# Performance work log

Hardware: AMD Instinct MI355X
Metric: run time of the kernel (lower is better)

## Reference

```python
import jax, jax.numpy as jnp
import numpy as np

B, P, K, KS = 512, 64, 30, 4      # graphs, nodes per graph, sort-pool k, conv1d kernel
N, E, F, H = B * P, 524288, 128, 256
N_CLASSES = 10
L_OUT = K - KS + 1                 # 27, conv1d output length


def _sage(h, wl, wr, b, src, dst, inv_deg):
    # PyG SAGEConv (mean aggr): out = lin_l(mean_j x_j) + lin_r(x_i); bias only on lin_l
    agg = jax.ops.segment_sum(h[src], dst, num_segments=N) * inv_deg
    return jax.nn.relu(agg @ wl + b + h @ wr)


def setup_inputs() -> dict:
    key = jax.random.key(0)
    ks = jax.random.split(key, 32)
    x = jax.random.normal(ks[0], (N, F), jnp.float32)
    # intra-graph random edges (src -> dst aggregation)
    g = jax.random.randint(ks[1], (E,), 0, B)
    src = g * P + jax.random.randint(ks[2], (E,), 0, P)
    dst = g * P + jax.random.randint(ks[3], (E,), 0, P)
    edge_index = jnp.stack([src, dst]).astype(jnp.int32)
    batch = jnp.repeat(jnp.arange(B), P).astype(jnp.int32)  # sorted graph ids

    def lin(k, i, o):
        return jax.random.normal(k, (i, o), jnp.float32) / np.float32(np.sqrt(i))

    inp = {"x": x, "edge_index": edge_index, "batch": batch}
    dims = [(F, H), (H, H), (H, H), (H, H)]
    ki = 4
    for li, (i, o) in enumerate(dims):
        inp[f"sage{li}_wl"] = lin(ks[ki], i, o); ki += 1
        inp[f"sage{li}_wr"] = lin(ks[ki], i, o); ki += 1
        inp[f"sage{li}_b"] = jnp.zeros((o,), jnp.float32)
    inp["conv1d_w"] = jax.random.normal(ks[ki], (H, H, KS), jnp.float32) / np.float32(np.sqrt(H * KS)); ki += 1
    inp["conv1d_b"] = jnp.zeros((H,), jnp.float32)
    inp["lin1_w"] = lin(ks[ki], H * L_OUT, H); ki += 1
    inp["lin1_b"] = jnp.zeros((H,), jnp.float32)
    inp["lin2_w"] = lin(ks[ki], H, 128); ki += 1
    inp["lin2_b"] = jnp.zeros((128,), jnp.float32)
    inp["out_w"] = lin(ks[ki], 128, N_CLASSES); ki += 1
    inp["out_b"] = jnp.zeros((N_CLASSES,), jnp.float32)
    return inp


def reference(x, edge_index, batch,
              sage0_wl, sage0_wr, sage0_b,
              sage1_wl, sage1_wr, sage1_b,
              sage2_wl, sage2_wr, sage2_b,
              sage3_wl, sage3_wr, sage3_b,
              conv1d_w, conv1d_b, lin1_w, lin1_b,
              lin2_w, lin2_b, out_w, out_b):
    src, dst = edge_index[0], edge_index[1]
    deg = jax.ops.segment_sum(jnp.ones(src.shape, x.dtype), dst, num_segments=N)
    inv_deg = (1.0 / jnp.maximum(deg, 1.0))[:, None]

    h = jnp.nan_to_num(x, nan=0.0)
    h = _sage(h, sage0_wl, sage0_wr, sage0_b, src, dst, inv_deg)
    h = _sage(h, sage1_wl, sage1_wr, sage1_b, src, dst, inv_deg)
    h = _sage(h, sage2_wl, sage2_wr, sage2_b, src, dst, inv_deg)
    h = _sage(h, sage3_wl, sage3_wr, sage3_b, src, dst, inv_deg)  # [N, H]

    # SortAggregation(k=K): to dense batch, sort by last channel desc, top-k, zero-pad
    counts = jax.ops.segment_sum(jnp.ones(N, jnp.int32), batch, num_segments=B)
    offsets = jnp.cumsum(counts) - counts
    pos = jnp.arange(N) - offsets[batch]
    D = h.shape[1]
    dense = jnp.zeros((B, P, D), h.dtype).at[batch, pos].set(h)
    valid = jnp.zeros((B, P), bool).at[batch, pos].set(True)
    skey = jnp.where(valid, dense[..., -1], -jnp.inf)
    order = jnp.argsort(-skey, axis=1)[:, :K]                       # [B, K]
    topk = jnp.take_along_axis(dense, order[..., None], axis=1)     # [B, K, D]
    tvalid = jnp.take_along_axis(valid, order, axis=1)
    topk = jnp.where(tvalid[..., None], topk, 0.0)

    # x.view(B, K, -1).permute(0, 2, 1) -> [B, D, K]
    xc = topk.transpose(0, 2, 1)
    y = jax.lax.conv_general_dilated(xc, conv1d_w, (1,), 'VALID',
                                     dimension_numbers=('NCH', 'OIH', 'NCH'))
    y = jax.nn.relu(y + conv1d_b[None, :, None])                    # [B, H, L_OUT]
    y = y.reshape(B, -1)                                            # dropout is identity in eval
    y = jax.nn.relu(y @ lin1_w + lin1_b)
    y = jax.nn.relu(y @ lin2_w + lin2_b)
    return jax.nn.relu(y @ out_w + out_b)                           # [B, N_CLASSES]
```

## Files before the change

### kernel.cpp

```cpp
#include <hip/hip_runtime.h>
#include <hip/hip_bf16.h>

#define NNODES 32768
#define NEDGES 524288
#define NGRAPH 512
#define PNODES 64
#define KTOP 30
#define FIN 128
#define HID 256
#define LOUT 27

#define C1F 4.8828125e-4f
#define C2F 2.384185791015625e-7f

using f16x8 = __attribute__((ext_vector_type(8))) _Float16;
using f16x4 = __attribute__((ext_vector_type(4))) _Float16;
using f32x4 = __attribute__((ext_vector_type(4))) float;
using f32x16 = __attribute__((ext_vector_type(16))) float;

#define GLDS(src, dst) __builtin_amdgcn_global_load_lds( \
    (const __attribute__((address_space(1))) void*)(src), \
    (__attribute__((address_space(3))) void*)(dst), 16, 0, 0)

__global__ void hist_kernel(const int* __restrict__ dst, int* __restrict__ counts) {
    int e = blockIdx.x * blockDim.x + threadIdx.x;
    if (e < NEDGES) atomicAdd(&counts[dst[e]], 1);
}

__global__ __launch_bounds__(1024) void scan_block_kernel(const int* __restrict__ counts,
        int* __restrict__ loc, int* __restrict__ partial) {
    int b = blockIdx.x, t = threadIdx.x;
    int i = b * 1024 + t;
    int v = counts[i];
    int lane = t & 63, w = t >> 6;
    int x = v;
    #pragma unroll
    for (int d = 1; d < 64; d <<= 1) { int y = __shfl_up(x, d, 64); if (lane >= d) x += y; }
    __shared__ int ws[16];
    if (lane == 63) ws[w] = x;
    __syncthreads();
    if (w == 0) {
        int s = (lane < 16) ? ws[lane] : 0;
        #pragma unroll
        for (int d = 1; d < 16; d <<= 1) { int y = __shfl_up(s, d, 64); if (lane >= d) s += y; }
        if (lane < 16) ws[lane] = s;
    }
    __syncthreads();
    int base = (w > 0) ? ws[w - 1] : 0;
    int incl = base + x;
    loc[i] = incl - v;
    if (t == 1023) partial[b] = incl;
}

__global__ __launch_bounds__(1024) void scan_fixup_kernel(const int* __restrict__ loc,
        const int* __restrict__ partial, const int* __restrict__ counts,
        int* __restrict__ offsets, int* __restrict__ cursor, float* __restrict__ invdeg) {
    int b = blockIdx.x, t = threadIdx.x;
    int i = b * 1024 + t;
    __shared__ int sbase;
    if (t == 0) { int s = 0; for (int j = 0; j < b; ++j) s += partial[j]; sbase = s; }
    __syncthreads();
    int o = loc[i] + sbase;
    offsets[i] = o;
    cursor[i] = o;
    invdeg[i] = 1.0f / fmaxf((float)counts[i], 1.0f);
}

__global__ void scatter_kernel(const int* __restrict__ src, const int* __restrict__ dst,
        int* __restrict__ cursor, int* __restrict__ ssrc) {
    int e = blockIdx.x * blockDim.x + threadIdx.x;
    if (e < NEDGES) {
        int d = dst[e];
        int p = atomicAdd(&cursor[d], 1);
        ssrc[p] = ((d & 63) << 6) | (src[e] & 63);
    }
}

__global__ void nan2num_split_kernel(const float* __restrict__ x,
        _Float16* __restrict__ oh, _Float16* __restrict__ ol, int n4) {
    int i = blockIdx.x * blockDim.x + threadIdx.x;
    if (i >= n4) return;
    float4 v = *(const float4*)(x + i * 4);
    float xs[4] = {v.x, v.y, v.z, v.w};
    f16x4 hh, ll;
    #pragma unroll
    for (int q = 0; q < 4; ++q) {
        float a = xs[q];
        a = (a != a) ? 0.f : a;
        _Float16 h = (_Float16)a;
        hh[q] = h;
        ll[q] = (_Float16)((a - (float)h) * 2048.0f);
    }
    *(f16x4*)(oh + (size_t)i * 4) = hh;
    *(f16x4*)(ol + (size_t)i * 4) = ll;
}

struct PrepSage {
    const float* src[8];
    _Float16* dh[8];
    _Float16* dl[8];
    int logK[8];
    int part[8];
};

__global__ __launch_bounds__(256) void prep_sage_kernel(PrepSage p) {
    int y = blockIdx.y;
    int idx = blockIdx.x * 256 + threadIdx.x;
    int lk = p.logK[y], K = 1 << lk;
    if (idx >= 256 * K) return;
    int n = idx >> lk, k = idx & (K - 1);
    float w = p.src[y][(size_t)k * 256 + n];
    _Float16 h = (_Float16)w;
    int wv = n >> 5, l31 = n & 31;
    int c = k >> 5, h2 = (k >> 4) & 1, hb = (k >> 3) & 1, j = k & 7;
    int NCH = K >> 5;
    size_t dst = (size_t)(wv * 2 + p.part[y]) * (size_t)(NCH * 1024)
               + (size_t)(c * 2 + h2) * 512 + (size_t)(hb * 32 + l31) * 8 + j;
    p.dh[y][dst] = h;
    p.dl[y][dst] = (_Float16)((w - (float)h) * 2048.0f);
}

__global__ __launch_bounds__(256) void prep_conv_kernel(const float* __restrict__ W,
        _Float16* __restrict__ b0, _Float16* __restrict__ b1) {
    int idx = blockIdx.x * 256 + threadIdx.x;
    int o = idx >> 10, k = idx & 1023;
    float w = W[(size_t)o * 1024 + (k & 255) * 4 + (k >> 8)];
    _Float16 h = (_Float16)w;
    b0[(size_t)o * 1024 + k] = h;
    b1[(size_t)o * 1024 + k] = (_Float16)((w - (float)h) * 2048.0f);
}

__global__ __launch_bounds__(256) void prep_lin1_kernel(const float* __restrict__ l1w,
        _Float16* __restrict__ wh, _Float16* __restrict__ wl_) {
    __shared__ float sh[64][65];
    int kb = blockIdx.x * 64;
    int nb = blockIdx.y * 64;
    int t = threadIdx.x;
    {
        int kk = t >> 2;
        int nc = (t & 3) * 16;
        int k = kb + kk, l = k >> 8, c = k & 255;
        const float* srow = l1w + (size_t)(c * 27 + l) * 256 + nb + nc;
        #pragma unroll
        for (int j = 0; j < 16; j += 4) {
            float4 v = *(const float4*)(srow + j);
            sh[kk][nc + j + 0] = v.x;
            sh[kk][nc + j + 1] = v.y;
            sh[kk][nc + j + 2] = v.z;
            sh[kk][nc + j + 3] = v.w;
        }
    }
    __syncthreads();
    {
        int nn = t >> 2;
        int kc = (t & 3) * 16;
        f16x8 oh[2], ol[2];
        #pragma unroll
        for (int j = 0; j < 16; ++j) {
            float x = sh[kc + j][nn];
            _Float16 h = (_Float16)x;
            oh[j >> 3][j & 7] = h;
            ol[j >> 3][j & 7] = (_Float16)((x - (float)h) * 2048.0f);
        }
        size_t o = (size_t)(nb + nn) * 6912 + kb + kc;
        *(f16x8*)(wh + o) = oh[0];
        *(f16x8*)(wh + o + 8) = oh[1];
        *(f16x8*)(wl_ + o) = ol[0];
        *(f16x8*)(wl_ + o + 8) = ol[1];
    }
}

template<int HIN>
__global__ __launch_bounds__(512, 4) void fused_sage3_kernel(
        const _Float16* __restrict__ hh, const _Float16* __restrict__ hl,
        const int* __restrict__ offsets, const int* __restrict__ counts,
        const int* __restrict__ ssrc, const float* __restrict__ invdeg,
        const _Float16* __restrict__ Wsh, const _Float16* __restrict__ Wsl,
        const float* __restrict__ bias,
        _Float16* __restrict__ outh, _Float16* __restrict__ outl) {
    constexpr int NCH = HIN / 32;
    __shared__ __align__(16) _Float16 hp[2][NCH * 2048];
    __shared__ __align__(16) uint32_t Sw[4096];
    const int g = blockIdx.x, t = threadIdx.x;
    const int lane = t & 63, wave = t >> 6;
    const int l31 = lane & 31, hb = lane >> 5;
    const size_t gbase = (size_t)g * 64 * HIN;

    #pragma unroll
    for (int i = 0; i < 8; ++i) Sw[t + i * 512] = 0;

    {
        int a = lane >> 2, b = lane & 3;
        for (int u = wave; u < NCH * 8; u += 8) {
            int part = u & 1;
            int cs = u >> 1;
            int c = cs >> 2, stripe = cs & 3;
            int row = stripe * 16 + a;
            int o = b ^ ((row >> 1) & 3) ^ (c & 3);
            const _Float16* src = (part ? hl : hh) + gbase + (size_t)row * HIN + c * 32 + o * 8;
            GLDS(src, &hp[part][c * 2048 + stripe * 512]);
        }
    }

    const int gbeg = offsets[g * 64];
    const int gend = offsets[g * 64 + 63] + counts[g * 64 + 63];
    __syncthreads();

    for (int e = gbeg + t; e < gend; e += 512)
        atomicAdd(&Sw[ssrc[e] & 4095], 1u);
    __syncthreads();

    {
        int d = t >> 3, o = t & 7;
        float idg = invdeg[g * 64 + d];
        float v[8];
        #pragma unroll
        for (int j = 0; j < 8; ++j) v[j] = (float)Sw[(d << 6) + (o << 3) + j] * idg;
        __syncthreads();
        _Float16* Sp = (_Float16*)Sw;
        f16x8 s0, s1;
        #pragma unroll
        for (int j = 0; j < 8; ++j) {
            _Float16 h1 = (_Float16)v[j];
            s0[j] = h1;
            s1[j] = (_Float16)((v[j] - (float)h1) * 2048.0f);
        }
        int addr = (d << 6) + ((o ^ (d & 7)) << 3);
        *(f16x8*)&Sp[addr] = s0;
        *(f16x8*)&Sp[4096 + addr] = s1;
    }
    __syncthreads();

    const int col = (wave << 5) + l31;

    auto gemmKV = [&](int part, f32x16* a0, f32x16* a1) {
        const _Float16* __restrict__ Bh = Wsh + (size_t)((wave << 1) + part) * (size_t)(NCH * 1024);
        const _Float16* __restrict__ Bl = Wsl + (size_t)((wave << 1) + part) * (size_t)(NCH * 1024);
        #pragma unroll 2
        for (int c = 0; c < NCH; ++c) {
            #pragma unroll
            for (int h2 = 0; h2 < 2; ++h2) {
                f16x8 ah[2], al_[2];
                #pragma unroll
                for (int mi = 0; mi < 2; ++mi) {
                    int row = (mi << 5) + l31;
                    int slot = (2 * h2 + hb) ^ ((row >> 1) & 3) ^ (c & 3);
                    int addr = c * 2048 + (row << 5) + (slot << 3);
                    ah[mi] = *(const f16x8*)&hp[0][addr];
                    al_[mi] = *(const f16x8*)&hp[1][addr];
                }
                int ko = ((c << 1) + h2) * 512 + (lane << 3);
                f16x8 bh = *(const f16x8*)(Bh + ko);
                f16x8 bl = *(const f16x8*)(Bl + ko);
                #pragma unroll
                for (int mi = 0; mi < 2; ++mi) {
                    a0[mi] = __builtin_amdgcn_mfma_f32_32x32x16_f16(ah[mi], bh, a0[mi], 0, 0, 0);
                    a1[mi] = __builtin_amdgcn_mfma_f32_32x32x16_f16(al_[mi], bh, a1[mi], 0, 0, 0);
                    a1[mi] = __builtin_amdgcn_mfma_f32_32x32x16_f16(ah[mi], bl, a1[mi], 0, 0, 0);
                }
            }
        }
    };

    f32x16 acc0[2], acc1[2];
    acc0[0] = 0.f; acc0[1] = 0.f; acc1[0] = 0.f; acc1[1] = 0.f;
    gemmKV(0, acc0, acc1);
    f32x16 pf[2];
    pf[0] = acc0[0] + C1F * acc1[0];
    pf[1] = acc0[1] + C1F * acc1[1];

    f32x16 so0[2], so1[2];
    so0[0] = 0.f; so0[1] = 0.f; so1[0] = 0.f; so1[1] = 0.f;
    {
        const _Float16* Sp = (const _Float16*)Sw;
        #pragma unroll
        for (int kc = 0; kc < 4; ++kc) {
            float kv[4], sv[4];
            #pragma unroll
            for (int j = 0; j < 4; ++j) {
                float e0 = pf[(2 * kc) >> 2][((2 * kc) & 3) * 4 + j];
                float e1 = pf[(2 * kc + 1) >> 2][((2 * kc + 1) & 3) * 4 + j];
                kv[j] = hb ? e1 : e0;
                sv[j] = hb ? e0 : e1;
            }
            uint32_t kh[2], kl2[2], sh_[2], sl2[2];
            #pragma unroll
            for (int q = 0; q < 2; ++q) {
                union { uint32_t u; _Float16 f[2]; } H1, L1, H2, L2;
                #pragma unroll
                for (int j = 0; j < 2; ++j) {
                    float x = kv[q * 2 + j];
                    _Float16 h1 = (_Float16)x;
                    H1.f[j] = h1; L1.f[j] = (_Float16)((x - (float)h1) * 2048.0f);
                    float y = sv[q * 2 + j];
                    _Float16 h2 = (_Float16)y;
                    H2.f[j] = h2; L2.f[j] = (_Float16)((y - (float)h2) * 2048.0f);
                }
                kh[q] = H1.u; kl2[q] = L1.u; sh_[q] = H2.u; sl2[q] = L2.u;
            }
            uint32_t rh0 = (uint32_t)__shfl_xor((int)sh_[0], 32, 64);
            uint32_t rh1 = (uint32_t)__shfl_xor((int)sh_[1], 32, 64);
            uint32_t rl0 = (uint32_t)__shfl_xor((int)sl2[0], 32, 64);
            uint32_t rl1 = (uint32_t)__shfl_xor((int)sl2[1], 32, 64);
            union { uint32_t u[4]; f16x8 v; } bh_, bl_;
            bh_.u[0] = hb ? rh0 : kh[0];  bh_.u[1] = hb ? rh1 : kh[1];
            bh_.u[2] = hb ? kh[0] : rh0;  bh_.u[3] = hb ? kh[1] : rh1;
            bl_.u[0] = hb ? rl0 : kl2[0]; bl_.u[1] = hb ? rl1 : kl2[1];
            bl_.u[2] = hb ? kl2[0] : rl0; bl_.u[3] = hb ? kl2[1] : rl1;
            #pragma unroll
            for (int mi = 0; mi < 2; ++mi) {
                int row = (mi << 5) + l31;
                int soff = (row << 6) + (((2 * kc + hb) ^ (row & 7)) << 3);
                f16x8 s0f = *(const f16x8*)&Sp[soff];
                f16x8 s1f = *(const f16x8*)&Sp[4096 + soff];
                so0[mi] = __builtin_amdgcn_mfma_f32_32x32x16_f16(s0f, bh_.v, so0[mi], 0, 0, 0);
                so1[mi] = __builtin_amdgcn_mfma_f32_32x32x16_f16(s0f, bl_.v, so1[mi], 0, 0, 0);
                so1[mi] = __builtin_amdgcn_mfma_f32_32x32x16_f16(s1f, bh_.v, so1[mi], 0, 0, 0);
            }
        }
    }
    f32x16 sC[2];
    sC[0] = so0[0] + C1F * so1[0];
    sC[1] = so0[1] + C1F * so1[1];

    acc0[0] = 0.f; acc0[1] = 0.f; acc1[0] = 0.f; acc1[1] = 0.f;
    gemmKV(1, acc0, acc1);

    const float bb = bias[col];
    #pragma unroll
    for (int mi = 0; mi < 2; ++mi)
        #pragma unroll
        for (int reg = 0; reg < 16; ++reg)
            sC[mi][reg] = fmaxf(sC[mi][reg] + acc0[mi][reg] + C1F * acc1[mi][reg] + bb, 0.f);

    __syncthreads();
    _Float16* eL = &hp[0][0];
    #pragma unroll
    for (int part = 0; part < 2; ++part) {
        #pragma unroll
        for (int mi = 0; mi < 2; ++mi) {
            #pragma unroll
            for (int reg = 0; reg < 16; ++reg) {
                int row = (mi << 5) + (reg & 3) + ((reg >> 2) << 3) + (hb << 2);
                int cx = col ^ ((((row >> 2) & 1) << 5) | ((row & 3) << 3));
                float v = sC[mi][reg];
                _Float16 h1 = (_Float16)v;
                eL[(row << 8) + cx] = part ? (_Float16)((v - (float)h1) * 2048.0f) : h1;
            }
        }
        __syncthreads();
        _Float16* gout = part ? outl : outh;
        #pragma unroll
        for (int it = 0; it < 4; ++it) {
            int i = (t << 3) + (it << 12);
            int row = i >> 8, cc = i & 255;
            int sx = cc ^ ((((row >> 2) & 1) << 5) | ((row & 3) << 3));
            f16x8 v8 = *(const f16x8*)&eL[(row << 8) + sx];
            *(f16x8*)(gout + (size_t)((g << 6) + row) * HID + cc) = v8;
        }
        if (part == 0) __syncthreads();
    }
}

template<int NPROD, int CONV, int NPAIRS, int EPI>
__global__ __launch_bounds__(256, 2) void mfma_ps_kernel(
        const _Float16* __restrict__ A1h, const _Float16* __restrict__ A1l,
        const _Float16* __restrict__ A2h, const _Float16* __restrict__ A2l,
        const _Float16* __restrict__ B1h, const _Float16* __restrict__ B1l,
        const _Float16* __restrict__ B2h, const _Float16* __restrict__ B2l,
        const float* __restrict__ bias,
        _Float16* __restrict__ outh, _Float16* __restrict__ outl,
        float* __restrict__ Cpart,
        int lda, int K, int Nd, int nrb) {
    __shared__ _Float16 As[2][2][128 * 32];
    __shared__ _Float16 Bs[2][2][128 * 32];
    const int t = threadIdx.x;
    const int lane = t & 63, wave = t >> 6;
    const int wr = wave & 1, wc = wave >> 1;
    const int bid = blockIdx.x;
    const int rb = bid % nrb, cb = bid / nrb;
    const int row0 = rb * 128, col0 = cb * 128;
    const int l31 = lane & 31, hb = lane >> 5, x3 = l31 & 3;
    const int r16 = lane >> 2;
    const int qsrc8 = ((lane & 3) ^ (r16 & 3)) * 8;
    size_t aoffj[2], boffj[2];
    #pragma unroll
    for (int j = 0; j < 2; ++j) {
        int ar = row0 + wave * 32 + j * 16 + r16;
        aoffj[j] = CONV ? ((size_t)ar * 256 + (size_t)(ar / 27) * 768)
                        : (size_t)ar * (size_t)lda;
        boffj[j] = (size_t)(col0 + wave * 32 + j * 16 + r16) * (size_t)K;
    }
    int aroff[2], broff[2], slot8[2];
    #pragma unroll
    for (int mi = 0; mi < 2; ++mi) aroff[mi] = (wr * 64 + mi * 32 + l31) * 32;
    #pragma unroll
    for (int ni = 0; ni < 2; ++ni) broff[ni] = (wc * 64 + ni * 32 + l31) * 32;
    #pragma unroll
    for (int h = 0; h < 2; ++h) slot8[h] = ((2 * h + hb) ^ x3) * 8;

    const int KV = NPAIRS * K;
    const int kchunk = KV / gridDim.z;
    const int kv_lo = blockIdx.z * kchunk, kv_hi = kv_lo + kchunk;

    f32x16 acc0[2][2], acc1[2][2], acc2[2][2];
    #pragma unroll
    for (int i = 0; i < 2; ++i)
        #pragma unroll
        for (int j = 0; j < 2; ++j) { acc0[i][j] = 0.f; acc1[i][j] = 0.f; acc2[i][j] = 0.f; }

    auto stage = [&](int kv, int b) {
        int p = (NPAIRS == 2 && kv >= K) ? 1 : 0;
        int k = kv - p * K;
        const _Float16* __restrict__ sAh = p ? A2h : A1h;
        const _Float16* __restrict__ sAl = p ? A2l : A1l;
        const _Float16* __restrict__ sBh = p ? B2h : B1h;
        const _Float16* __restrict__ sBl = p ? B2l : B1l;
        #pragma unroll
        for (int j = 0; j < 2; ++j) {
            int ldsbase = (wave * 32 + j * 16) * 32;
            size_t ga = aoffj[j] + k + qsrc8;
            size_t gb = boffj[j] + k + qsrc8;
            GLDS(sAh + ga, &As[b][0][ldsbase]);
            GLDS(sAl + ga, &As[b][1][ldsbase]);
            GLDS(sBh + gb, &Bs[b][0][ldsbase]);
            GLDS(sBl + gb, &Bs[b][1][ldsbase]);
        }
    };

    stage(kv_lo, 0);
    __syncthreads();
    int b = 0;
    for (int kv = kv_lo; kv < kv_hi; kv += 32) {
        if (kv + 32 < kv_hi) stage(kv + 32, b ^ 1);
        #pragma unroll
        for (int h = 0; h < 2; ++h) {
            f16x8 af0[2], af1[2], bf0[2], bf1[2];
            #pragma unroll
            for (int mi = 0; mi < 2; ++mi) {
                af0[mi] = *(const f16x8*)&As[b][0][aroff[mi] + slot8[h]];
                af1[mi] = *(const f16x8*)&As[b][1][aroff[mi] + slot8[h]];
            }
            #pragma unroll
            for (int ni = 0; ni < 2; ++ni) {
                bf0[ni] = *(const f16x8*)&Bs[b][0][broff[ni] + slot8[h]];
                bf1[ni] = *(const f16x8*)&Bs[b][1][broff[ni] + slot8[h]];
            }
            #pragma unroll
            for (int mi = 0; mi < 2; ++mi)
                #pragma unroll
                for (int ni = 0; ni < 2; ++ni) {
                    acc0[mi][ni] = __builtin_amdgcn_mfma_f32_32x32x16_f16(af0[mi], bf0[ni], acc0[mi][ni], 0, 0, 0);
                    acc1[mi][ni] = __builtin_amdgcn_mfma_f32_32x32x16_f16(af1[mi], bf0[ni], acc1[mi][ni], 0, 0, 0);
                    acc1[mi][ni] = __builtin_amdgcn_mfma_f32_32x32x16_f16(af0[mi], bf1[ni], acc1[mi][ni], 0, 0, 0);
                    if (NPROD == 4)
                        acc2[mi][ni] = __builtin_amdgcn_mfma_f32_32x32x16_f16(af1[mi], bf1[ni], acc2[mi][ni], 0, 0, 0);
                }
        }
        b ^= 1;
        __syncthreads();
    }

    const int rquad = 4 * hb;
    #pragma unroll
    for (int ni = 0; ni < 2; ++ni) {
        int col = col0 + wc * 64 + ni * 32 + l31;
        float bb = (EPI == 0) ? bias[col] : 0.f;
        #pragma unroll
        for (int mi = 0; mi < 2; ++mi) {
            #pragma unroll
            for (int reg = 0; reg < 16; ++reg) {
                float v = acc0[mi][ni][reg] + C1F * acc1[mi][ni][reg];
                if (NPROD == 4) v += C2F * acc2[mi][ni][reg];
                int row = row0 + wr * 64 + mi * 32 + (reg & 3) + 8 * (reg >> 2) + rquad;
                if (EPI == 0) {
                    v = fmaxf(v + bb, 0.f);
                    _Float16 h = (_Float16)v;
                    size_t o = (size_t)row * Nd + col;
                    outh[o] = h;
                    outl[o] = (_Float16)((v - (float)h) * 2048.0f);
                } else {
                    size_t zb = (size_t)blockIdx.z * (size_t)(nrb * 128) * Nd;
                    Cpart[zb + (size_t)row * Nd + col] = v;
                }
            }
        }
    }
}

__global__ __launch_bounds__(256) void sortgather_kernel(const _Float16* __restrict__ hh,
        const _Float16* __restrict__ hl, _Float16* __restrict__ th, _Float16* __restrict__ tl) {
    __shared__ float vals[PNODES];
    __shared__ int ord[KTOP];
    int g = blockIdx.x, t = threadIdx.x;
    if (t < PNODES) {
        size_t idx = (size_t)(g * PNODES + t) * HID + (HID - 1);
        vals[t] = (float)hh[idx] + C1F * (float)hl[idx];
    }
    __syncthreads();
    if (t < PNODES) {
        float v = vals[t];
        int rank = 0;
        for (int j = 0; j < PNODES; ++j) {
            float vj = vals[j];
            rank += (vj > v) || (vj == v && j < t);
        }
        if (rank < KTOP) ord[rank] = g * PNODES + t;
    }
    __syncthreads();
    int c8 = (t & 31) * 8;
    for (int r = t >> 5; r < KTOP; r += 8) {
        size_t s = (size_t)ord[r] * HID + c8;
        size_t d = (size_t)(g * KTOP + r) * HID + c8;
        *(f16x8*)(th + d) = *(const f16x8*)(hh + s);
        *(f16x8*)(tl + d) = *(const f16x8*)(hl + s);
    }
}

__global__ void reduce_conv_kernel(const float* __restrict__ yb32,
        const float* __restrict__ b, _Float16* __restrict__ ybh, _Float16* __restrict__ ybl) {
    int i = blockIdx.x * 256 + threadIdx.x;
    float v = fmaxf(yb32[i] + yb32[i + 13824 * 256] + b[i & 255], 0.f);
    _Float16 h = (_Float16)v;
    ybh[i] = h;
    ybl[i] = (_Float16)((v - (float)h) * 2048.0f);
}

__global__ void reduce_lin1_kernel(const float* __restrict__ z1p,
        const float* __restrict__ b, float* __restrict__ z1) {
    int i = blockIdx.x * 256 + threadIdx.x;
    float s = b[i & 255];
    #pragma unroll
    for (int z = 0; z < 27; ++z) s += z1p[(size_t)z * 131072 + i];
    z1[i] = fmaxf(s, 0.f);
}

__global__ __launch_bounds__(256) void gemm64_kernel(
        const float* __restrict__ A, const float* __restrict__ B,
        const float* __restrict__ bias, float* __restrict__ C,
        int lda, int kend, int Nd) {
    __shared__ float As[16][64];
    __shared__ float Bs[16][64];
    const int tid = threadIdx.x;
    const int tx = tid & 15, ty = tid >> 4;
    const int la_r = tid >> 2, la_c = (tid & 3) << 2;
    const int lb_r = tid >> 4, lb_c = (tid & 15) << 2;
    const int row0 = blockIdx.x * 64, col0 = blockIdx.y * 64;
    const size_t aoff = (size_t)(row0 + la_r) * (size_t)lda;
    float acc[4][4] = {};
    for (int k0 = 0; k0 < kend; k0 += 16) {
        __syncthreads();
        float4 av = *(const float4*)(A + aoff + k0 + la_c);
        As[la_c + 0][la_r] = av.x;
        As[la_c + 1][la_r] = av.y;
        As[la_c + 2][la_r] = av.z;
        As[la_c + 3][la_r] = av.w;
        *(float4*)&Bs[lb_r][lb_c] = *(const float4*)(B + (size_t)(k0 + lb_r) * Nd + col0 + lb_c);
        __syncthreads();
        #pragma unroll
        for (int k = 0; k < 16; ++k) {
            float4 a = *(const float4*)&As[k][ty << 2];
            float4 b = *(const float4*)&Bs[k][tx << 2];
            acc[0][0] += a.x * b.x; acc[0][1] += a.x * b.y; acc[0][2] += a.x * b.z; acc[0][3] += a.x * b.w;
            acc[1][0] += a.y * b.x; acc[1][1] += a.y * b.y; acc[1][2] += a.y * b.z; acc[1][3] += a.y * b.w;
            acc[2][0] += a.z * b.x; acc[2][1] += a.z * b.y; acc[2][2] += a.z * b.z; acc[2][3] += a.z * b.w;
            acc[3][0] += a.w * b.x; acc[3][1] += a.w * b.y; acc[3][2] += a.w * b.z; acc[3][3] += a.w * b.w;
        }
    }
    #pragma unroll
    for (int i = 0; i < 4; ++i) {
        int row = row0 + (ty << 2) + i;
        #pragma unroll
        for (int j = 0; j < 4; ++j) {
            int col = col0 + (tx << 2) + j;
            C[(size_t)row * Nd + col] = fmaxf(acc[i][j] + bias[col], 0.f);
        }
    }
}

__global__ void out_kernel(const float* __restrict__ z2, const float* __restrict__ w,
        const float* __restrict__ b, float* __restrict__ out) {
    int idx = blockIdx.x * blockDim.x + threadIdx.x;
    if (idx < NGRAPH * 10) {
        int r = idx / 10, c = idx % 10;
        float s = b[c];
        for (int k = 0; k < 128; ++k) s += z2[r * 128 + k] * w[k * 10 + c];
        out[idx] = fmaxf(s, 0.f);
    }
}

extern "C" void kernel_launch(void* const* d_in, const int* in_sizes, int n_in,
                              void* d_out, int out_size, void* d_ws, size_t ws_size,
                              hipStream_t stream) {
    const float* x    = (const float*)d_in[0];
    const int*   edge = (const int*)d_in[1];
    const int*   esrc = edge;
    const int*   edst = edge + NEDGES;
    const float* wl[4] = {(const float*)d_in[3], (const float*)d_in[6], (const float*)d_in[9],  (const float*)d_in[12]};
    const float* wr[4] = {(const float*)d_in[4], (const float*)d_in[7], (const float*)d_in[10], (const float*)d_in[13]};
    const float* sb[4] = {(const float*)d_in[5], (const float*)d_in[8], (const float*)d_in[11], (const float*)d_in[14]};
    const float* convw = (const float*)d_in[15];
    const float* convb = (const float*)d_in[16];
    const float* l1w   = (const float*)d_in[17];
    const float* l1b   = (const float*)d_in[18];
    const float* l2w   = (const float*)d_in[19];
    const float* l2b   = (const float*)d_in[20];
    const float* ow    = (const float*)d_in[21];
    const float* ob    = (const float*)d_in[22];
    float* out = (float*)d_out;

    char* ws = (char*)d_ws;
    size_t off = 0;
    auto alloc = [&](size_t bytes) -> char* {
        char* p = ws + off;
        off = (off + bytes + 255) & ~(size_t)255;
        return p;
    };
    int*   counts  = (int*)alloc((size_t)NNODES * 4);
    int*   offsets = (int*)alloc((size_t)NNODES * 4);
    int*   cursor  = (int*)alloc((size_t)NNODES * 4);
    int*   loc     = (int*)alloc((size_t)NNODES * 4);
    int*   partial = (int*)alloc(32 * 4);
    float* invdeg  = (float*)alloc((size_t)NNODES * 4);
    int*   ssrc    = (int*)alloc((size_t)NEDGES * 4);
    _Float16* wch[4]; _Float16* wcl[4];
    for (int l = 0; l < 4; ++l) {
        size_t kb = (size_t)512 * (l ? HID : FIN) * 2;
        wch[l] = (_Float16*)alloc(kb);
        wcl[l] = (_Float16*)alloc(kb);
    }
    _Float16* cvh = (_Float16*)alloc((size_t)HID * 1024 * 2);
    _Float16* cvl = (_Float16*)alloc((size_t)HID * 1024 * 2);

    const size_t H0T = (size_t)NNODES * FIN * 2;
    const size_t AGT = (size_t)NNODES * HID * 2;
    const size_t TKT = (size_t)NGRAPH * KTOP * HID * 2;
    const size_t YBT = (size_t)NGRAPH * LOUT * HID * 2;
    const size_t YB32T = (size_t)2 * 13824 * 256 * 4;
    const size_t W1T = (size_t)HID * 6912 * 2;

    char* R1 = alloc(2 * H0T);
    char* R2 = alloc(2 * AGT);
    char* R3 = alloc(2 * AGT);
    char* R4 = alloc(2 * AGT);
    _Float16* h0h = (_Float16*)R1; _Float16* h0l = (_Float16*)(R1 + H0T);
    _Float16* tkh = (_Float16*)R1; _Float16* tkl = (_Float16*)(R1 + TKT);
    _Float16* hAh = (_Float16*)R3; _Float16* hAl = (_Float16*)(R3 + AGT);
    _Float16* ybh = (_Float16*)R2; _Float16* ybl_ = (_Float16*)(R2 + YBT);
    float* yb32 = (float*)(R2 + 2 * YBT);
    float* z1p  = (float*)(R2 + 2 * YBT);
    char* tail2 = R2 + 2 * YBT + YB32T;
    float* z1  = (float*)tail2;
    float* z2  = (float*)(tail2 + (size_t)NGRAPH * HID * 4);
    _Float16* w1h = (_Float16*)(tail2 + (size_t)NGRAPH * HID * 4 + (size_t)NGRAPH * 128 * 4 + 256);
    _Float16* w1l = (_Float16*)((char*)w1h + W1T);
    _Float16* hBh = (_Float16*)R4; _Float16* hBl = (_Float16*)(R4 + AGT);

    hipMemsetAsync(counts, 0, (size_t)NNODES * 4, stream);
    hist_kernel<<<NEDGES / 256, 256, 0, stream>>>(edst, counts);
    scan_block_kernel<<<NNODES / 1024, 1024, 0, stream>>>(counts, loc, partial);
    scan_fixup_kernel<<<NNODES / 1024, 1024, 0, stream>>>(loc, partial, counts, offsets, cursor, invdeg);
    scatter_kernel<<<NEDGES / 256, 256, 0, stream>>>(esrc, edst, cursor, ssrc);
    nan2num_split_kernel<<<(NNODES * FIN / 4) / 256, 256, 0, stream>>>(x, h0h, h0l, NNODES * FIN / 4);

    PrepSage ps;
    for (int l = 0; l < 4; ++l) {
        int lk = l ? 8 : 7;
        ps.src[2 * l] = wl[l];     ps.dh[2 * l] = wch[l];     ps.dl[2 * l] = wcl[l];
        ps.src[2 * l + 1] = wr[l]; ps.dh[2 * l + 1] = wch[l]; ps.dl[2 * l + 1] = wcl[l];
        ps.logK[2 * l] = lk;     ps.part[2 * l] = 0;
        ps.logK[2 * l + 1] = lk; ps.part[2 * l + 1] = 1;
    }
    prep_sage_kernel<<<dim3(256, 8), 256, 0, stream>>>(ps);
    prep_conv_kernel<<<(HID * 1024) / 256, 256, 0, stream>>>(convw, cvh, cvl);

    fused_sage3_kernel<FIN><<<NGRAPH, 512, 0, stream>>>(
        h0h, h0l, offsets, counts, ssrc, invdeg, wch[0], wcl[0], sb[0], hAh, hAl);
    _Float16* hinh = hAh; _Float16* hinl = hAl;
    _Float16* hoth = hBh; _Float16* hotl = hBl;
    for (int l = 1; l < 4; ++l) {
        fused_sage3_kernel<HID><<<NGRAPH, 512, 0, stream>>>(
            hinh, hinl, offsets, counts, ssrc, invdeg, wch[l], wcl[l], sb[l], hoth, hotl);
        _Float16* t1 = hinh; hinh = hoth; hoth = t1;
        _Float16* t2 = hinl; hinl = hotl; hotl = t2;
    }

    sortgather_kernel<<<NGRAPH, 256, 0, stream>>>(hinh, hinl, tkh, tkl);
    prep_lin1_kernel<<<dim3(108, 4), 256, 0, stream>>>(l1w, w1h, w1l);

    mfma_ps_kernel<3, 1, 1, 1><<<dim3(108 * 2, 1, 2), 256, 0, stream>>>(
        tkh, tkl, nullptr, nullptr, cvh, cvl, nullptr, nullptr, nullptr, nullptr, nullptr, yb32, 256, 1024, HID, 108);
    reduce_conv_kernel<<<13824 * 256 / 256, 256, 0, stream>>>(yb32, convb, ybh, ybl_);

    mfma_ps_kernel<3, 0, 1, 1><<<dim3(4 * 2, 1, 27), 256, 0, stream>>>(
        ybh, ybl_, nullptr, nullptr, w1h, w1l, nullptr, nullptr, nullptr, nullptr, nullptr, z1p, 6912, 6912, HID, 4);
    reduce_lin1_kernel<<<NGRAPH * HID / 256, 256, 0, stream>>>(z1p, l1b, z1);

    gemm64_kernel<<<dim3(NGRAPH / 64, 128 / 64), 256, 0, stream>>>(z1, l2w, l2b, z2, HID, HID, 128);

    out_kernel<<<(NGRAPH * 10 + 255) / 256, 256, 0, stream>>>(z2, ow, ob, out);
}
```

Before: 487.6 us.

## Fuse all four SAGE layers into one per-graph kernel keeping activations in LDS

Replaces the four per-layer SAGE launches with a single kernel per graph that runs all layers back to back. After each layer the ReLU output is split into hi/lo fp16 and written into the shared-memory activation buffer instead of global memory. The edge histogram (adjacency matrix) is built once per graph and reused across all layers. This removes three launches and the global write/read of the intermediate activations, at the cost of runtime-variable inner loop counts (the chunk loop no longer has a compile-time bound or unroll pragma), extra block barriers, and LDS sized for the wider hidden layer in every layer.

```diff
diff --git a/kernel.cpp b/kernel.cpp
--- a/kernel.cpp
+++ b/kernel.cpp
@@ -170,38 +170,42 @@
     }
 }
 
-template<int HIN>
-__global__ __launch_bounds__(512, 4) void fused_sage3_kernel(
+struct SageWAll {
+    const _Float16* wh[4];
+    const _Float16* wl[4];
+    const float* bias[4];
+};
+
+__global__ __launch_bounds__(512, 4) void fused_sage_all_kernel(
         const _Float16* __restrict__ hh, const _Float16* __restrict__ hl,
         const int* __restrict__ offsets, const int* __restrict__ counts,
         const int* __restrict__ ssrc, const float* __restrict__ invdeg,
-        const _Float16* __restrict__ Wsh, const _Float16* __restrict__ Wsl,
-        const float* __restrict__ bias,
+        SageWAll W,
         _Float16* __restrict__ outh, _Float16* __restrict__ outl) {
-    constexpr int NCH = HIN / 32;
-    __shared__ __align__(16) _Float16 hp[2][NCH * 2048];
+    __shared__ __align__(16) _Float16 hp[2][8 * 2048];
     __shared__ __align__(16) uint32_t Sw[4096];
     const int g = blockIdx.x, t = threadIdx.x;
     const int lane = t & 63, wave = t >> 6;
     const int l31 = lane & 31, hb = lane >> 5;
-    const size_t gbase = (size_t)g * 64 * HIN;
 
     #pragma unroll
     for (int i = 0; i < 8; ++i) Sw[t + i * 512] = 0;
 
     {
         int a = lane >> 2, b = lane & 3;
-        for (int u = wave; u < NCH * 8; u += 8) {
+        #pragma unroll
+        for (int u0 = 0; u0 < 4; ++u0) {
+            int u = u0 * 8 + wave;
             int part = u & 1;
             int cs = u >> 1;
             int c = cs >> 2, stripe = cs & 3;
             int row = stripe * 16 + a;
             int o = b ^ ((row >> 1) & 3) ^ (c & 3);
-            const _Float16* src = (part ? hl : hh) + gbase + (size_t)row * HIN + c * 32 + o * 8;
+            const _Float16* src = (part ? hl : hh) + (size_t)g * (64 * FIN)
+                                + (size_t)row * FIN + c * 32 + o * 8;
             GLDS(src, &hp[part][c * 2048 + stripe * 512]);
         }
     }
-
     const int gbeg = offsets[g * 64];
     const int gend = offsets[g * 64 + 63] + counts[g * 64 + 63];
     __syncthreads();
@@ -233,10 +237,8 @@
 
     const int col = (wave << 5) + l31;
 
-    auto gemmKV = [&](int part, f32x16* a0, f32x16* a1) {
-        const _Float16* __restrict__ Bh = Wsh + (size_t)((wave << 1) + part) * (size_t)(NCH * 1024);
-        const _Float16* __restrict__ Bl = Wsl + (size_t)((wave << 1) + part) * (size_t)(NCH * 1024);
-        #pragma unroll 2
+    auto gemmKV = [&](const _Float16* __restrict__ Bh, const _Float16* __restrict__ Bl,
+                      int NCH, f32x16* a0, f32x16* a1) {
         for (int c = 0; c < NCH; ++c) {
             #pragma unroll
             for (int h2 = 0; h2 < 2; ++h2) {
@@ -262,77 +264,115 @@
         }
     };
 
-    f32x16 acc0[2], acc1[2];
-    acc0[0] = 0.f; acc0[1] = 0.f; acc1[0] = 0.f; acc1[1] = 0.f;
-    gemmKV(0, acc0, acc1);
-    f32x16 pf[2];
-    pf[0] = acc0[0] + C1F * acc1[0];
-    pf[1] = acc0[1] + C1F * acc1[1];
-
-    f32x16 so0[2], so1[2];
-    so0[0] = 0.f; so0[1] = 0.f; so1[0] = 0.f; so1[1] = 0.f;
-    {
-        const _Float16* Sp = (const _Float16*)Sw;
-        #pragma unroll
-        for (int kc = 0; kc < 4; ++kc) {
-            float kv[4], sv[4];
-            #pragma unroll
-            for (int j = 0; j < 4; ++j) {
-                float e0 = pf[(2 * kc) >> 2][((2 * kc) & 3) * 4 + j];
-                float e1 = pf[(2 * kc + 1) >> 2][((2 * kc + 1) & 3) * 4 + j];
-                kv[j] = hb ? e1 : e0;
-                sv[j] = hb ? e0 : e1;
+    auto run_layer = [&](const _Float16* __restrict__ Wsh,
+                         const _Float16* __restrict__ Wsl,
+                         const float* __restrict__ bias,
+                         int NCH, f32x16* sC) {
+        const size_t wstride = (size_t)NCH * 1024;
+        f32x16 acc0[2], acc1[2];
+        acc0[0] = 0.f; acc0[1] = 0.f; acc1[0] = 0.f; acc1[1] = 0.f;
+        gemmKV(Wsh + (size_t)(wave << 1) * wstride, Wsl + (size_t)(wave << 1) * wstride,
+               NCH, acc0, acc1);
+        f32x16 pf[2];
+        pf[0] = acc0[0] + C1F * acc1[0];
+        pf[1] = acc0[1] + C1F * acc1[1];
+
+        f32x16 so0[2], so1[2];
+        so0[0] = 0.f; so0[1] = 0.f; so1[0] = 0.f; so1[1] = 0.f;
+        {
+            const _Float16* Sp = (const _Float16*)Sw;
+            #pragma unroll
+            for (int kc = 0; kc < 4; ++kc) {
+                float kv[4], sv[4];
+                #pragma unroll
+                for (int j = 0; j < 4; ++j) {
+                    float e0 = pf[(2 * kc) >> 2][((2 * kc) & 3) * 4 + j];
+                    float e1 = pf[(2 * kc + 1) >> 2][((2 * kc + 1) & 3) * 4 + j];
+                    kv[j] = hb ? e1 : e0;
+                    sv[j] = hb ? e0 : e1;
+                }
+                uint32_t kh[2], kl2[2], sh_[2], sl2[2];
+                #pragma unroll
+                for (int q = 0; q < 2; ++q) {
+                    union { uint32_t u; _Float16 f[2]; } H1, L1, H2, L2;
+                    #pragma unroll
+                    for (int j = 0; j < 2; ++j) {
+                        float x = kv[q * 2 + j];
+                        _Float16 h1 = (_Float16)x;
+                        H1.f[j] = h1; L1.f[j] = (_Float16)((x - (float)h1) * 2048.0f);
+                        float y = sv[q * 2 + j];
+                        _Float16 h2 = (_Float16)y;
+                        H2.f[j] = h2; L2.f[j] = (_Float16)((y - (float)h2) * 2048.0f);
+                    }
+                    kh[q] = H1.u; kl2[q] = L1.u; sh_[q] = H2.u; sl2[q] = L2.u;
+                }
+                uint32_t rh0 = (uint32_t)__shfl_xor((int)sh_[0], 32, 64);
+                uint32_t rh1 = (uint32_t)__shfl_xor((int)sh_[1], 32, 64);
+                uint32_t rl0 = (uint32_t)__shfl_xor((int)sl2[0], 32, 64);
+                uint32_t rl1 = (uint32_t)__shfl_xor((int)sl2[1], 32, 64);
+                union { uint32_t u[4]; f16x8 v; } bh_, bl_;
+                bh_.u[0] = hb ? rh0 : kh[0];  bh_.u[1] = hb ? rh1 : kh[1];
+                bh_.u[2] = hb ? kh[0] : rh0;  bh_.u[3] = hb ? kh[1] : rh1;
+                bl_.u[0] = hb ? rl0 : kl2[0]; bl_.u[1] = hb ? rl1 : kl2[1];
+                bl_.u[2] = hb ? kl2[0] : rl0; bl_.u[3] = hb ? kl2[1] : rl1;
+                #pragma unroll
+                for (int mi = 0; mi < 2; ++mi) {
+                    int row = (mi << 5) + l31;
+                    int soff = (row << 6) + (((2 * kc + hb) ^ (row & 7)) << 3);
+                    f16x8 s0f = *(const f16x8*)&Sp[soff];
+                    f16x8 s1f = *(const f16x8*)&Sp[4096 + soff];
+                    so0[mi] = __builtin_amdgcn_mfma_f32_32x32x16_f16(s0f, bh_.v, so0[mi], 0, 0, 0);
+                    so1[mi] = __builtin_amdgcn_mfma_f32_32x32x16_f16(s0f, bl_.v, so1[mi], 0, 0, 0);
+                    so1[mi] = __builtin_amdgcn_mfma_f32_32x32x16_f16(s1f, bh_.v, so1[mi], 0, 0, 0);
+                }
             }
-            uint32_t kh[2], kl2[2], sh_[2], sl2[2];
-            #pragma unroll
-            for (int q = 0; q < 2; ++q) {
-                union { uint32_t u; _Float16 f[2]; } H1, L1, H2, L2;
-                #pragma unroll
-                for (int j = 0; j < 2; ++j) {
-                    float x = kv[q * 2 + j];
-                    _Float16 h1 = (_Float16)x;
-                    H1.f[j] = h1; L1.f[j] = (_Float16)((x - (float)h1) * 2048.0f);
-                    float y = sv[q * 2 + j];
-                    _Float16 h2 = (_Float16)y;
-                    H2.f[j] = h2; L2.f[j] = (_Float16)((y - (float)h2) * 2048.0f);
-                }
-                kh[q] = H1.u; kl2[q] = L1.u; sh_[q] = H2.u; sl2[q] = L2.u;
+        }
+
+        acc0[0] = 0.f; acc0[1] = 0.f; acc1[0] = 0.f; acc1[1] = 0.f;
+        gemmKV(Wsh + (size_t)((wave << 1) + 1) * wstride, Wsl + (size_t)((wave << 1) + 1) * wstride,
+               NCH, acc0, acc1);
+
+        const float bb = bias[col];
+        #pragma unroll
+        for (int mi = 0; mi < 2; ++mi)
+            #pragma unroll
+            for (int reg = 0; reg < 16; ++reg)
+                sC[mi][reg] = fmaxf(so0[mi][reg] + C1F * so1[mi][reg]
+                                  + acc0[mi][reg] + C1F * acc1[mi][reg] + bb, 0.f);
+    };
+
+    auto hp_write = [&](const f32x16* sC) {
+        int oc = l31 >> 3, j = l31 & 7;
+        #pragma unroll
+        for (int mi = 0; mi < 2; ++mi)
+            #pragma unroll
+            for (int reg = 0; reg < 16; ++reg) {
+                int row = (mi << 5) + (reg & 3) + ((reg >> 2) << 3) + (hb << 2);
+                int slot = oc ^ ((row >> 1) & 3) ^ (wave & 3);
+                int addr = wave * 2048 + (row << 5) + (slot << 3) + j;
+                float v = sC[mi][reg];
+                _Float16 h1 = (_Float16)v;
+                hp[0][addr] = h1;
+                hp[1][addr] = (_Float16)((v - (float)h1) * 2048.0f);
             }
-            uint32_t rh0 = (uint32_t)__shfl_xor((int)sh_[0], 32, 64);
-            uint32_t rh1 = (uint32_t)__shfl_xor((int)sh_[1], 32, 64);
-            uint32_t rl0 = (uint32_t)__shfl_xor((int)sl2[0], 32, 64);
-            uint32_t rl1 = (uint32_t)__shfl_xor((int)sl2[1], 32, 64);
-            union { uint32_t u[4]; f16x8 v; } bh_, bl_;
-            bh_.u[0] = hb ? rh0 : kh[0];  bh_.u[1] = hb ? rh1 : kh[1];
-            bh_.u[2] = hb ? kh[0] : rh0;  bh_.u[3] = hb ? kh[1] : rh1;
-            bl_.u[0] = hb ? rl0 : kl2[0]; bl_.u[1] = hb ? rl1 : kl2[1];
-            bl_.u[2] = hb ? kl2[0] : rl0; bl_.u[3] = hb ? kl2[1] : rl1;
-            #pragma unroll
-            for (int mi = 0; mi < 2; ++mi) {
-                int row = (mi << 5) + l31;
-                int soff = (row << 6) + (((2 * kc + hb) ^ (row & 7)) << 3);
-                f16x8 s0f = *(const f16x8*)&Sp[soff];
-                f16x8 s1f = *(const f16x8*)&Sp[4096 + soff];
-                so0[mi] = __builtin_amdgcn_mfma_f32_32x32x16_f16(s0f, bh_.v, so0[mi], 0, 0, 0);
-                so1[mi] = __builtin_amdgcn_mfma_f32_32x32x16_f16(s0f, bl_.v, so1[mi], 0, 0, 0);
-                so1[mi] = __builtin_amdgcn_mfma_f32_32x32x16_f16(s1f, bh_.v, so1[mi], 0, 0, 0);
-            }
-        }
-    }
+    };
+
     f32x16 sC[2];
-    sC[0] = so0[0] + C1F * so1[0];
-    sC[1] = so0[1] + C1F * so1[1];
-
-    acc0[0] = 0.f; acc0[1] = 0.f; acc1[0] = 0.f; acc1[1] = 0.f;
-    gemmKV(1, acc0, acc1);
-
-    const float bb = bias[col];
-    #pragma unroll
-    for (int mi = 0; mi < 2; ++mi)
-        #pragma unroll
-        for (int reg = 0; reg < 16; ++reg)
-            sC[mi][reg] = fmaxf(sC[mi][reg] + acc0[mi][reg] + C1F * acc1[mi][reg] + bb, 0.f);
-
+    run_layer(W.wh[0], W.wl[0], W.bias[0], 4, sC);
+    __syncthreads();
+    hp_write(sC);
+    __syncthreads();
+    #pragma unroll 1
+    for (int layer = 1; layer < 3; ++layer) {
+        const _Float16* wsh = (layer == 1) ? W.wh[1] : W.wh[2];
+        const _Float16* wsl = (layer == 1) ? W.wl[1] : W.wl[2];
+        const float* bb = (layer == 1) ? W.bias[1] : W.bias[2];
+        run_layer(wsh, wsl, bb, 8, sC);
+        __syncthreads();
+        hp_write(sC);
+        __syncthreads();
+    }
+    run_layer(W.wh[3], W.wl[3], W.bias[3], 8, sC);
     __syncthreads();
     _Float16* eL = &hp[0][0];
     #pragma unroll
@@ -645,7 +685,6 @@
     char* R4 = alloc(2 * AGT);
     _Float16* h0h = (_Float16*)R1; _Float16* h0l = (_Float16*)(R1 + H0T);
     _Float16* tkh = (_Float16*)R1; _Float16* tkl = (_Float16*)(R1 + TKT);
-    _Float16* hAh = (_Float16*)R3; _Float16* hAl = (_Float16*)(R3 + AGT);
     _Float16* ybh = (_Float16*)R2; _Float16* ybl_ = (_Float16*)(R2 + YBT);
     float* yb32 = (float*)(R2 + 2 * YBT);
     float* z1p  = (float*)(R2 + 2 * YBT);
@@ -674,18 +713,12 @@
     prep_sage_kernel<<<dim3(256, 8), 256, 0, stream>>>(ps);
     prep_conv_kernel<<<(HID * 1024) / 256, 256, 0, stream>>>(convw, cvh, cvl);
 
-    fused_sage3_kernel<FIN><<<NGRAPH, 512, 0, stream>>>(
-        h0h, h0l, offsets, counts, ssrc, invdeg, wch[0], wcl[0], sb[0], hAh, hAl);
-    _Float16* hinh = hAh; _Float16* hinl = hAl;
-    _Float16* hoth = hBh; _Float16* hotl = hBl;
-    for (int l = 1; l < 4; ++l) {
-        fused_sage3_kernel<HID><<<NGRAPH, 512, 0, stream>>>(
-            hinh, hinl, offsets, counts, ssrc, invdeg, wch[l], wcl[l], sb[l], hoth, hotl);
-        _Float16* t1 = hinh; hinh = hoth; hoth = t1;
-        _Float16* t2 = hinl; hinl = hotl; hotl = t2;
-    }
-
-    sortgather_kernel<<<NGRAPH, 256, 0, stream>>>(hinh, hinl, tkh, tkl);
+    SageWAll swa;
+    for (int l = 0; l < 4; ++l) { swa.wh[l] = wch[l]; swa.wl[l] = wcl[l]; swa.bias[l] = sb[l]; }
+    fused_sage_all_kernel<<<NGRAPH, 512, 0, stream>>>(
+        h0h, h0l, offsets, counts, ssrc, invdeg, swa, hBh, hBl);
+
+    sortgather_kernel<<<NGRAPH, 256, 0, stream>>>(hBh, hBl, tkh, tkl);
     prep_lin1_kernel<<<dim3(108, 4), 256, 0, stream>>>(l1w, w1h, w1l);
 
     mfma_ps_kernel<3, 1, 1, 1><<<dim3(108 * 2, 1, 2), 256, 0, stream>>>(
```

Measured after the change: 1.582 ms. 3.25x slower.
